# Kernel optimization log

Measured on AMD Instinct MI355X. Metric: run time of the kernel, lower is better.

The kernel has to match this reference:

```python
import jax, jax.numpy as jnp
import numpy as np

EMB = 1024
HEADS = 16
HEAD_DIM = EMB // HEADS


def setup_inputs() -> dict:
    key = jax.random.key(0)
    k1, k2, k3, k4 = jax.random.split(key, 4)
    x = jax.random.normal(k1, (4, 2048, EMB), dtype=jnp.float32)
    # torch Linear weight is [out, in]; store as [in, out] for x @ W
    W_qkv = jax.random.normal(k2, (EMB, 3 * EMB), dtype=jnp.float32) * (1.0 / np.sqrt(EMB))
    W_proj = jax.random.normal(k3, (EMB, EMB), dtype=jnp.float32) * (1.0 / np.sqrt(EMB))
    b_proj = jax.random.normal(k4, (EMB,), dtype=jnp.float32) * 0.01
    return {"x": x, "W_qkv": W_qkv, "W_proj": W_proj, "b_proj": b_proj}


def reference(x, W_qkv, W_proj, b_proj):
    B, S, D = x.shape
    H, hd = HEADS, HEAD_DIM
    qkv = x @ W_qkv                                  # [B,S,3D]
    q, k, v = jnp.split(qkv, 3, axis=-1)
    q = q.reshape(B, S, H, hd).transpose(0, 2, 1, 3)  # [B,H,S,hd]
    k = k.reshape(B, S, H, hd).transpose(0, 2, 1, 3)
    v = v.reshape(B, S, H, hd).transpose(0, 2, 1, 3)
    att = jnp.einsum('bhqd,bhkd->bhqk', q, k) * (1.0 / np.sqrt(hd))
    causal = jnp.tril(jnp.ones((S, S), dtype=bool))
    att = jnp.where(causal[None, None], att, jnp.float32(-jnp.inf))
    att = jax.nn.softmax(att, axis=-1)
    # dropout omitted (eval mode / deterministic baseline)
    out = jnp.einsum('bhqk,bhkd->bhqd', att, v)       # [B,H,S,hd]
    out = out.transpose(0, 2, 1, 3).reshape(B, S, D)
    return out @ W_proj + b_proj
```

## Files before the change

### kernel.cpp

```cpp
#include <hip/hip_runtime.h>
#include <math.h>

#define S_   2048
#define D_   1024
#define H_   16
#define HD_  64
#define BH_  64
#define TOK_ 8192

typedef __attribute__((ext_vector_type(8))) short  short8;
typedef __attribute__((ext_vector_type(4))) float  floatx4;

__device__ __forceinline__ short f2bf(float f) {
  union { float f; unsigned u; } c; c.f = f;
  unsigned u = c.u;
  u += 0x7fffu + ((u >> 16) & 1u);
  return (short)(u >> 16);
}

__device__ __forceinline__ void gload16(const void* g, void* l) {
  __builtin_amdgcn_global_load_lds((const __attribute__((address_space(1))) void*)g,
                                   (__attribute__((address_space(3))) void*)l, 16, 0, 0);
}

__global__ void cvt_x_kernel(const float* __restrict__ in, short* __restrict__ out, int n8) {
  int i = blockIdx.x * blockDim.x + threadIdx.x;
  if (i >= n8) return;
  const float4* p = (const float4*)in;
  float4 a = p[i * 2], b = p[i * 2 + 1];
  short8 o;
  o[0] = f2bf(a.x); o[1] = f2bf(a.y); o[2] = f2bf(a.z); o[3] = f2bf(a.w);
  o[4] = f2bf(b.x); o[5] = f2bf(b.y); o[6] = f2bf(b.z); o[7] = f2bf(b.w);
  ((short8*)out)[i] = o;
}

__global__ void tconv_kernel(const float* __restrict__ in, short* __restrict__ out, int R, int C) {
  __shared__ float t[32][33];
  int tx = threadIdx.x, ty = threadIdx.y;
  int c0 = blockIdx.x * 32, r0 = blockIdx.y * 32;
#pragma unroll
  for (int i = 0; i < 4; ++i)
    t[ty + i * 8][tx] = in[(r0 + ty + i * 8) * C + c0 + tx];
  __syncthreads();
#pragma unroll
  for (int i = 0; i < 4; ++i)
    out[(c0 + ty + i * 8) * R + r0 + tx] = f2bf(t[tx][ty + i * 8]);
}

__global__ void tv_kernel(const short* __restrict__ vb, short* __restrict__ vtb) {
  __shared__ short t[32][33];
  int tx = threadIdx.x, ty = threadIdx.y;
  int bh = blockIdx.z;
  int d0 = blockIdx.x * 32, s0 = blockIdx.y * 32;
  const short* src = vb + bh * S_ * HD_;
  short* dst = vtb + bh * HD_ * S_;
#pragma unroll
  for (int i = 0; i < 4; ++i)
    t[ty + i * 8][tx] = src[(s0 + ty + i * 8) * HD_ + d0 + tx];
  __syncthreads();
#pragma unroll
  for (int i = 0; i < 4; ++i)
    dst[(d0 + ty + i * 8) * S_ + s0 + tx] = t[tx][ty + i * 8];
}

__global__ __launch_bounds__(256) void gemm_qkv_kernel(
    const short* __restrict__ A, const short* __restrict__ Bt,
    short* __restrict__ qb, short* __restrict__ kb, short* __restrict__ vb) {
  __shared__ short sA[128 * 32];
  __shared__ short sB[128 * 32];
  const int tid = threadIdx.x;
  const int lane = tid & 63, wid = tid >> 6;
  const int wm = wid >> 1, wn = wid & 1;
  const int lr = lane & 15, lg = lane >> 4;
  const int m0 = blockIdx.x * 128, n0 = blockIdx.y * 128;
  floatx4 acc[4][4] = {};
  const int f1 = tid * 16;
  const int rS1 = f1 >> 6, cS1 = (f1 & 63) >> 1;
  const int f2 = f1 + 4096;
  const int rS2 = f2 >> 6, cS2 = (f2 & 63) >> 1;
  for (int kt = 0; kt < 32; ++kt) {
    const int k0 = kt * 32;
    __syncthreads();
    gload16(&A[(m0 + rS1) * 1024 + k0 + cS1], (char*)sA + f1);
    gload16(&A[(m0 + rS2) * 1024 + k0 + cS2], (char*)sA + f2);
    gload16(&Bt[(n0 + rS1) * 1024 + k0 + cS1], (char*)sB + f1);
    gload16(&Bt[(n0 + rS2) * 1024 + k0 + cS2], (char*)sB + f2);
    __syncthreads();
    short8 af[4], bfv[4];
#pragma unroll
    for (int mf = 0; mf < 4; ++mf)
      af[mf] = *(const short8*)&sA[(wm * 64 + mf * 16 + lr) * 32 + lg * 8];
#pragma unroll
    for (int nf = 0; nf < 4; ++nf)
      bfv[nf] = *(const short8*)&sB[(wn * 64 + nf * 16 + lr) * 32 + lg * 8];
#pragma unroll
    for (int mf = 0; mf < 4; ++mf)
#pragma unroll
      for (int nf = 0; nf < 4; ++nf)
        acc[mf][nf] = __builtin_amdgcn_mfma_f32_16x16x32_bf16(af[mf], bfv[nf], acc[mf][nf], 0, 0, 0);
  }
  const int sec = n0 >> 10;
  short* dst = sec == 0 ? qb : (sec == 1 ? kb : vb);
  const float scale = (sec == 0) ? 0.18033688011112042f : 1.0f;
#pragma unroll
  for (int mf = 0; mf < 4; ++mf) {
#pragma unroll
    for (int nf = 0; nf < 4; ++nf) {
      const int col = n0 + wn * 64 + nf * 16 + lr;
      const int w = col & 1023;
      const int h = w >> 6, d = w & 63;
#pragma unroll
      for (int r = 0; r < 4; ++r) {
        const int token = m0 + wm * 64 + mf * 16 + lg * 4 + r;
        const int b = token >> 11, s = token & 2047;
        dst[(((b << 4) | h) * 2048 + s) * 64 + d] = f2bf(acc[mf][nf][r] * scale);
      }
    }
  }
}

__global__ __launch_bounds__(256) void gemm_proj_kernel(
    const short* __restrict__ A, const short* __restrict__ Bt,
    const float* __restrict__ bias, float* __restrict__ out) {
  __shared__ short sA[128 * 32];
  __shared__ short sB[128 * 32];
  const int tid = threadIdx.x;
  const int lane = tid & 63, wid = tid >> 6;
  const int wm = wid >> 1, wn = wid & 1;
  const int lr = lane & 15, lg = lane >> 4;
  const int m0 = blockIdx.x * 128, n0 = blockIdx.y * 128;
  floatx4 acc[4][4] = {};
  const int f1 = tid * 16;
  const int rS1 = f1 >> 6, cS1 = (f1 & 63) >> 1;
  const int f2 = f1 + 4096;
  const int rS2 = f2 >> 6, cS2 = (f2 & 63) >> 1;
  for (int kt = 0; kt < 32; ++kt) {
    const int k0 = kt * 32;
    __syncthreads();
    gload16(&A[(m0 + rS1) * 1024 + k0 + cS1], (char*)sA + f1);
    gload16(&A[(m0 + rS2) * 1024 + k0 + cS2], (char*)sA + f2);
    gload16(&Bt[(n0 + rS1) * 1024 + k0 + cS1], (char*)sB + f1);
    gload16(&Bt[(n0 + rS2) * 1024 + k0 + cS2], (char*)sB + f2);
    __syncthreads();
    short8 af[4], bfv[4];
#pragma unroll
    for (int mf = 0; mf < 4; ++mf)
      af[mf] = *(const short8*)&sA[(wm * 64 + mf * 16 + lr) * 32 + lg * 8];
#pragma unroll
    for (int nf = 0; nf < 4; ++nf)
      bfv[nf] = *(const short8*)&sB[(wn * 64 + nf * 16 + lr) * 32 + lg * 8];
#pragma unroll
    for (int mf = 0; mf < 4; ++mf)
#pragma unroll
      for (int nf = 0; nf < 4; ++nf)
        acc[mf][nf] = __builtin_amdgcn_mfma_f32_16x16x32_bf16(af[mf], bfv[nf], acc[mf][nf], 0, 0, 0);
  }
#pragma unroll
  for (int mf = 0; mf < 4; ++mf) {
#pragma unroll
    for (int nf = 0; nf < 4; ++nf) {
      const int col = n0 + wn * 64 + nf * 16 + lr;
      const float bv = bias[col];
#pragma unroll
      for (int r = 0; r < 4; ++r) {
        const int row = m0 + wm * 64 + mf * 16 + lg * 4 + r;
        out[row * 1024 + col] = acc[mf][nf][r] + bv;
      }
    }
  }
}

__global__ __launch_bounds__(256) void attn_kernel(
    const short* __restrict__ qb, const short* __restrict__ kb,
    const short* __restrict__ vtb, short* __restrict__ attb) {
  __shared__ short sK[2][64 * 64];
  __shared__ short sVT[2][64 * 64];
  __shared__ short sP[4][32 * 64];
  const int tid = threadIdx.x;
  const int lane = tid & 63, wid = tid >> 6;
  const int lr = lane & 15, lg = lane >> 4;

  const int bid = blockIdx.x;
  const int wgid = (bid & 7) * 64 + (bid >> 3);
  const int bh = wgid >> 3;
  const int qx = wgid & 7;

  const char* kbase = (const char*)(kb + bh * S_ * HD_);
  const char* vtbase = (const char*)(vtb + bh * HD_ * S_);
  const short* qbase = qb + bh * S_ * HD_;
  char* pbase = (char*)&sP[wid][0];
  const int b = bh >> 4, h = bh & 15;

  const int f1 = tid * 16;
  const int ro1 = f1 >> 7, cb1 = f1 & 127;
  const int sc1 = cb1 ^ ((ro1 & 7) << 4);
  const int f2 = f1 + 4096;
  const int ro2 = f2 >> 7, cb2 = f2 & 127;
  const int sc2 = cb2 ^ ((ro2 & 7) << 4);

  const int swz = (lr & 7) << 4;

  short8 vones;
#pragma unroll
  for (int j = 0; j < 8; ++j) vones[j] = (short)0x3F80;

#pragma unroll 1
  for (int half = 0; half < 2; ++half) {
    const int qt = half ? (15 - qx) : qx;
    const int qw = qt * 128 + wid * 32;

    short8 qf[2][2];
#pragma unroll
    for (int qtile = 0; qtile < 2; ++qtile)
#pragma unroll
      for (int kf = 0; kf < 2; ++kf)
        qf[qtile][kf] = *(const short8*)&qbase[(qw + qtile * 16 + lr) * 64 + kf * 32 + lg * 8];

    floatx4 acc_o[2][4] = {};
    floatx4 acc_den[2] = {};
    float mrun[2] = {-1e30f, -1e30f};

    const int ntiles = 2 * qt + 2;

    {
      char* dK = (char*)sK[0];
      char* dV = (char*)sVT[0];
      gload16(kbase + ro1 * 128 + sc1, dK + f1);
      gload16(kbase + ro2 * 128 + sc2, dK + f2);
      gload16(vtbase + ro1 * 4096 + sc1, dV + f1);
      gload16(vtbase + ro2 * 4096 + sc2, dV + f2);
      asm volatile("s_waitcnt vmcnt(0)" ::: "memory");
      __builtin_amdgcn_s_barrier();
      __builtin_amdgcn_sched_barrier(0);
    }

    int cur = 0;
#pragma unroll 1
    for (int t = 0; t < ntiles; ++t) {
      if (t + 1 < ntiles) {
        const int key0n = (t + 1) * 64;
        char* dK = (char*)sK[cur ^ 1];
        char* dV = (char*)sVT[cur ^ 1];
        gload16(kbase + (key0n + ro1) * 128 + sc1, dK + f1);
        gload16(kbase + (key0n + ro2) * 128 + sc2, dK + f2);
        gload16(vtbase + ro1 * 4096 + key0n * 2 + sc1, dV + f1);
        gload16(vtbase + ro2 * 4096 + key0n * 2 + sc2, dV + f2);
      }
      const int key0 = t * 64;
      if (key0 <= qw + 31) {
        const char* cK = (const char*)sK[cur];
        const char* cV = (const char*)sVT[cur];

        floatx4 sT[4][2] = {};
        __builtin_amdgcn_s_setprio(1);
#pragma unroll
        for (int kt = 0; kt < 4; ++kt) {
#pragma unroll
          for (int kf = 0; kf < 2; ++kf) {
            short8 kfrag = *(const short8*)(cK + (kt * 16 + lr) * 128 + ((kf * 64 + lg * 16) ^ swz));
#pragma unroll
            for (int qtile = 0; qtile < 2; ++qtile)
              sT[kt][qtile] = __builtin_amdgcn_mfma_f32_16x16x32_bf16(kfrag, qf[qtile][kf], sT[kt][qtile], 0, 0, 0);
          }
        }
        __builtin_amdgcn_s_setprio(0);

        if (key0 + 63 > qw) {
#pragma unroll
          for (int kt = 0; kt < 4; ++kt)
#pragma unroll
            for (int qtile = 0; qtile < 2; ++qtile)
#pragma unroll
              for (int r = 0; r < 4; ++r)
                if (key0 + kt * 16 + lg * 4 + r > qw + qtile * 16 + lr) sT[kt][qtile][r] = -1e30f;
        }

        float mx[2], al[2];
        bool need = false;
#pragma unroll
        for (int qtile = 0; qtile < 2; ++qtile) {
          float m0v = fmaxf(fmaxf(sT[0][qtile][0], sT[0][qtile][1]), fmaxf(sT[0][qtile][2], sT[0][qtile][3]));
          float m1v = fmaxf(fmaxf(sT[1][qtile][0], sT[1][qtile][1]), fmaxf(sT[1][qtile][2], sT[1][qtile][3]));
          float m2v = fmaxf(fmaxf(sT[2][qtile][0], sT[2][qtile][1]), fmaxf(sT[2][qtile][2], sT[2][qtile][3]));
          float m3v = fmaxf(fmaxf(sT[3][qtile][0], sT[3][qtile][1]), fmaxf(sT[3][qtile][2], sT[3][qtile][3]));
          float m = fmaxf(fmaxf(m0v, m1v), fmaxf(m2v, m3v));
          m = fmaxf(m, __shfl_xor(m, 16));
          m = fmaxf(m, __shfl_xor(m, 32));
          mx[qtile] = m;
          need = need || (m > mrun[qtile] + 8.f);
        }
        if (__any(need)) {
#pragma unroll
          for (int qtile = 0; qtile < 2; ++qtile) {
            const float mnew = fmaxf(mrun[qtile], mx[qtile]);
            al[qtile] = __builtin_amdgcn_exp2f(mrun[qtile] - mnew);
            mrun[qtile] = mnew;
          }
#pragma unroll
          for (int mf = 0; mf < 2; ++mf) {
#pragma unroll
            for (int r = 0; r < 4; ++r) {
              const float alr = __shfl(al[mf], lg * 4 + r);
              acc_den[mf][r] *= alr;
#pragma unroll
              for (int nfd = 0; nfd < 4; ++nfd) acc_o[mf][nfd][r] *= alr;
            }
          }
        }

#pragma unroll
        for (int kt = 0; kt < 4; ++kt) {
#pragma unroll
          for (int qtile = 0; qtile < 2; ++qtile) {
            const float p0 = __builtin_amdgcn_exp2f(sT[kt][qtile][0] - mrun[qtile]);
            const float p1 = __builtin_amdgcn_exp2f(sT[kt][qtile][1] - mrun[qtile]);
            const float p2 = __builtin_amdgcn_exp2f(sT[kt][qtile][2] - mrun[qtile]);
            const float p3 = __builtin_amdgcn_exp2f(sT[kt][qtile][3] - mrun[qtile]);
            unsigned lo, hi;
            asm("v_cvt_pk_bf16_f32 %0, %1, %2" : "=v"(lo) : "v"(p0), "v"(p1));
            asm("v_cvt_pk_bf16_f32 %0, %1, %2" : "=v"(hi) : "v"(p2), "v"(p3));
            *(unsigned long long*)(pbase + (qtile * 16 + lr) * 128 + ((kt * 32 + lg * 8) ^ swz)) =
                ((unsigned long long)hi << 32) | lo;
          }
        }

        __builtin_amdgcn_s_setprio(1);
#pragma unroll
        for (int kf2 = 0; kf2 < 2; ++kf2) {
          short8 pf[2];
#pragma unroll
          for (int mf = 0; mf < 2; ++mf) {
            pf[mf] = *(const short8*)(pbase + (mf * 16 + lr) * 128 + ((kf2 * 64 + lg * 16) ^ swz));
            acc_den[mf] = __builtin_amdgcn_mfma_f32_16x16x32_bf16(pf[mf], vones, acc_den[mf], 0, 0, 0);
          }
#pragma unroll
          for (int nfd = 0; nfd < 4; ++nfd) {
            short8 vfrag = *(const short8*)(cV + (nfd * 16 + lr) * 128 + ((kf2 * 64 + lg * 16) ^ swz));
#pragma unroll
            for (int mf = 0; mf < 2; ++mf)
              acc_o[mf][nfd] = __builtin_amdgcn_mfma_f32_16x16x32_bf16(pf[mf], vfrag, acc_o[mf][nfd], 0, 0, 0);
          }
        }
        __builtin_amdgcn_s_setprio(0);
      }

      __builtin_amdgcn_sched_barrier(0);
      asm volatile("s_waitcnt vmcnt(0)" ::: "memory");
      __builtin_amdgcn_s_barrier();
      __builtin_amdgcn_sched_barrier(0);
      cur ^= 1;
    }

#pragma unroll
    for (int mf = 0; mf < 2; ++mf) {
#pragma unroll
      for (int nfd = 0; nfd < 4; ++nfd) {
#pragma unroll
        for (int r = 0; r < 4; ++r) {
          const float o = acc_o[mf][nfd][r] / acc_den[mf][r];
          const int qrow = qw + mf * 16 + lg * 4 + r;
          const int d = nfd * 16 + lr;
          attb[(b * 2048 + qrow) * 1024 + h * 64 + d] = f2bf(o);
        }
      }
    }
  }
}

extern "C" void kernel_launch(void* const* d_in, const int* in_sizes, int n_in,
                              void* d_out, int out_size, void* d_ws, size_t ws_size,
                              hipStream_t stream) {
  (void)in_sizes; (void)n_in; (void)out_size; (void)ws_size;
  const float* x = (const float*)d_in[0];
  const float* Wqkv = (const float*)d_in[1];
  const float* Wproj = (const float*)d_in[2];
  const float* bproj = (const float*)d_in[3];
  float* out = (float*)d_out;

  char* w = (char*)d_ws;
  short* xb     = (short*)(w + 0);
  short* wqkvT  = (short*)(w + 16777216);
  short* wprojT = (short*)(w + 23068672);
  short* qb     = (short*)(w + 25165824);
  short* kb     = (short*)(w + 41943040);
  short* vb     = (short*)(w + 58720256);
  short* vtb    = (short*)(w + 75497472);
  short* attb   = (short*)(w + 92274688);

  cvt_x_kernel<<<4096, 256, 0, stream>>>(x, xb, TOK_ * D_ / 8);
  tconv_kernel<<<dim3(96, 32), dim3(32, 8), 0, stream>>>(Wqkv, wqkvT, 1024, 3072);
  tconv_kernel<<<dim3(32, 32), dim3(32, 8), 0, stream>>>(Wproj, wprojT, 1024, 1024);
  gemm_qkv_kernel<<<dim3(64, 24), 256, 0, stream>>>(xb, wqkvT, qb, kb, vb);
  tv_kernel<<<dim3(2, 64, 64), dim3(32, 8), 0, stream>>>(vb, vtb);
  attn_kernel<<<512, 256, 0, stream>>>(qb, kb, vtb, attb);
  gemm_proj_kernel<<<dim3(64, 8), 256, 0, stream>>>(attb, wprojT, bproj, out);
}
```

Before: 262.2 us.

## Fuse V transpose into QKV GEMM epilogue and triple-buffer attention K/V loads

The QKV GEMM now writes V directly in transposed layout, using packed 8-byte stores of four consecutive tokens, which removes the separate tv_kernel launch and its round trip through memory. The attention kernel moves from double to triple buffering of K/V tiles in LDS, waiting with vmcnt(4) so that one tile load stays in flight while the current tile is computed, and it drops the trailing barrier. The row-max reduction uses v_max3_f32 to cut the instruction count. Costs are more LDS per block, which may lower occupancy, and a fragile hand-tuned wait count.

New measurement: 264.7 us. No clear change (+0.9%).

```diff
diff --git a/kernel.cpp b/kernel.cpp
--- a/kernel.cpp
+++ b/kernel.cpp
@@ -16,6 +16,10 @@
   unsigned u = c.u;
   u += 0x7fffu + ((u >> 16) & 1u);
   return (short)(u >> 16);
+}
+
+__device__ __forceinline__ float max3f(float a, float b, float c) {
+  float d; asm("v_max3_f32 %0, %1, %2, %3" : "=v"(d) : "v"(a), "v"(b), "v"(c)); return d;
 }
 
 __device__ __forceinline__ void gload16(const void* g, void* l) {
@@ -47,25 +51,9 @@
     out[(c0 + ty + i * 8) * R + r0 + tx] = f2bf(t[tx][ty + i * 8]);
 }
 
-__global__ void tv_kernel(const short* __restrict__ vb, short* __restrict__ vtb) {
-  __shared__ short t[32][33];
-  int tx = threadIdx.x, ty = threadIdx.y;
-  int bh = blockIdx.z;
-  int d0 = blockIdx.x * 32, s0 = blockIdx.y * 32;
-  const short* src = vb + bh * S_ * HD_;
-  short* dst = vtb + bh * HD_ * S_;
-#pragma unroll
-  for (int i = 0; i < 4; ++i)
-    t[ty + i * 8][tx] = src[(s0 + ty + i * 8) * HD_ + d0 + tx];
-  __syncthreads();
-#pragma unroll
-  for (int i = 0; i < 4; ++i)
-    dst[(d0 + ty + i * 8) * S_ + s0 + tx] = t[tx][ty + i * 8];
-}
-
 __global__ __launch_bounds__(256) void gemm_qkv_kernel(
     const short* __restrict__ A, const short* __restrict__ Bt,
-    short* __restrict__ qb, short* __restrict__ kb, short* __restrict__ vb) {
+    short* __restrict__ qb, short* __restrict__ kb, short* __restrict__ vtb) {
   __shared__ short sA[128 * 32];
   __shared__ short sB[128 * 32];
   const int tid = threadIdx.x;
@@ -100,20 +88,40 @@
         acc[mf][nf] = __builtin_amdgcn_mfma_f32_16x16x32_bf16(af[mf], bfv[nf], acc[mf][nf], 0, 0, 0);
   }
   const int sec = n0 >> 10;
-  short* dst = sec == 0 ? qb : (sec == 1 ? kb : vb);
-  const float scale = (sec == 0) ? 0.18033688011112042f : 1.0f;
-#pragma unroll
-  for (int mf = 0; mf < 4; ++mf) {
-#pragma unroll
-    for (int nf = 0; nf < 4; ++nf) {
-      const int col = n0 + wn * 64 + nf * 16 + lr;
-      const int w = col & 1023;
-      const int h = w >> 6, d = w & 63;
-#pragma unroll
-      for (int r = 0; r < 4; ++r) {
-        const int token = m0 + wm * 64 + mf * 16 + lg * 4 + r;
-        const int b = token >> 11, s = token & 2047;
-        dst[(((b << 4) | h) * 2048 + s) * 64 + d] = f2bf(acc[mf][nf][r] * scale);
+  if (sec < 2) {
+    short* dst = sec == 0 ? qb : kb;
+    const float scale = (sec == 0) ? 0.18033688011112042f : 1.0f;
+#pragma unroll
+    for (int mf = 0; mf < 4; ++mf) {
+#pragma unroll
+      for (int nf = 0; nf < 4; ++nf) {
+        const int col = n0 + wn * 64 + nf * 16 + lr;
+        const int w = col & 1023;
+        const int h = w >> 6, d = w & 63;
+#pragma unroll
+        for (int r = 0; r < 4; ++r) {
+          const int token = m0 + wm * 64 + mf * 16 + lg * 4 + r;
+          const int b = token >> 11, s = token & 2047;
+          dst[(((b << 4) | h) * 2048 + s) * 64 + d] = f2bf(acc[mf][nf][r] * scale);
+        }
+      }
+    }
+  } else {
+#pragma unroll
+    for (int mf = 0; mf < 4; ++mf) {
+      const int token0 = m0 + wm * 64 + mf * 16 + lg * 4;
+      const int bb = token0 >> 11, s0v = token0 & 2047;
+#pragma unroll
+      for (int nf = 0; nf < 4; ++nf) {
+        const int col = n0 + wn * 64 + nf * 16 + lr;
+        const int w = col & 1023;
+        const int h = w >> 6, d = w & 63;
+        union { unsigned long long u; short s[4]; } pk;
+        pk.s[0] = f2bf(acc[mf][nf][0]);
+        pk.s[1] = f2bf(acc[mf][nf][1]);
+        pk.s[2] = f2bf(acc[mf][nf][2]);
+        pk.s[3] = f2bf(acc[mf][nf][3]);
+        *(unsigned long long*)&vtb[((((bb << 4) | h) * 64 + d) << 11) + s0v] = pk.u;
       }
     }
   }
@@ -173,8 +181,8 @@
 __global__ __launch_bounds__(256) void attn_kernel(
     const short* __restrict__ qb, const short* __restrict__ kb,
     const short* __restrict__ vtb, short* __restrict__ attb) {
-  __shared__ short sK[2][64 * 64];
-  __shared__ short sVT[2][64 * 64];
+  __shared__ short sK[3][64 * 64];
+  __shared__ short sVT[3][64 * 64];
   __shared__ short sP[4][32 * 64];
   const int tid = threadIdx.x;
   const int lane = tid & 63, wid = tid >> 6;
@@ -222,30 +230,35 @@
 
     const int ntiles = 2 * qt + 2;
 
-    {
-      char* dK = (char*)sK[0];
-      char* dV = (char*)sVT[0];
-      gload16(kbase + ro1 * 128 + sc1, dK + f1);
-      gload16(kbase + ro2 * 128 + sc2, dK + f2);
-      gload16(vtbase + ro1 * 4096 + sc1, dV + f1);
-      gload16(vtbase + ro2 * 4096 + sc2, dV + f2);
-      asm volatile("s_waitcnt vmcnt(0)" ::: "memory");
+    __builtin_amdgcn_s_barrier();
+
+    const char* kp1 = kbase + ro1 * 128 + sc1;
+    const char* kp2 = kbase + ro2 * 128 + sc2;
+    const char* vp1 = vtbase + ro1 * 4096 + sc1;
+    const char* vp2 = vtbase + ro2 * 4096 + sc2;
+
+    gload16(kp1, (char*)sK[0] + f1);  gload16(kp2, (char*)sK[0] + f2);
+    gload16(vp1, (char*)sVT[0] + f1); gload16(vp2, (char*)sVT[0] + f2);
+    kp1 += 8192; kp2 += 8192; vp1 += 128; vp2 += 128;
+    gload16(kp1, (char*)sK[1] + f1);  gload16(kp2, (char*)sK[1] + f2);
+    gload16(vp1, (char*)sVT[1] + f1); gload16(vp2, (char*)sVT[1] + f2);
+    kp1 += 8192; kp2 += 8192; vp1 += 128; vp2 += 128;
+
+    int cur = 0, nxt2 = 2;
+#pragma unroll 1
+    for (int t = 0; t < ntiles; ++t) {
+      if (t < ntiles - 1) { asm volatile("s_waitcnt vmcnt(4)" ::: "memory"); }
+      else                { asm volatile("s_waitcnt vmcnt(0)" ::: "memory"); }
       __builtin_amdgcn_s_barrier();
       __builtin_amdgcn_sched_barrier(0);
-    }
-
-    int cur = 0;
-#pragma unroll 1
-    for (int t = 0; t < ntiles; ++t) {
-      if (t + 1 < ntiles) {
-        const int key0n = (t + 1) * 64;
-        char* dK = (char*)sK[cur ^ 1];
-        char* dV = (char*)sVT[cur ^ 1];
-        gload16(kbase + (key0n + ro1) * 128 + sc1, dK + f1);
-        gload16(kbase + (key0n + ro2) * 128 + sc2, dK + f2);
-        gload16(vtbase + ro1 * 4096 + key0n * 2 + sc1, dV + f1);
-        gload16(vtbase + ro2 * 4096 + key0n * 2 + sc2, dV + f2);
-      }
+      if (t + 2 < ntiles) {
+        char* dK = (char*)sK[nxt2];
+        char* dV = (char*)sVT[nxt2];
+        gload16(kp1, dK + f1);  gload16(kp2, dK + f2);
+        gload16(vp1, dV + f1);  gload16(vp2, dV + f2);
+      }
+      kp1 += 8192; kp2 += 8192; vp1 += 128; vp2 += 128;
+
       const int key0 = t * 64;
       if (key0 <= qw + 31) {
         const char* cK = (const char*)sK[cur];
@@ -279,11 +292,14 @@
         bool need = false;
 #pragma unroll
         for (int qtile = 0; qtile < 2; ++qtile) {
-          float m0v = fmaxf(fmaxf(sT[0][qtile][0], sT[0][qtile][1]), fmaxf(sT[0][qtile][2], sT[0][qtile][3]));
-          float m1v = fmaxf(fmaxf(sT[1][qtile][0], sT[1][qtile][1]), fmaxf(sT[1][qtile][2], sT[1][qtile][3]));
-          float m2v = fmaxf(fmaxf(sT[2][qtile][0], sT[2][qtile][1]), fmaxf(sT[2][qtile][2], sT[2][qtile][3]));
-          float m3v = fmaxf(fmaxf(sT[3][qtile][0], sT[3][qtile][1]), fmaxf(sT[3][qtile][2], sT[3][qtile][3]));
-          float m = fmaxf(fmaxf(m0v, m1v), fmaxf(m2v, m3v));
+          float m = max3f(sT[0][qtile][0], sT[0][qtile][1], sT[0][qtile][2]);
+          m = max3f(m, sT[0][qtile][3], sT[1][qtile][0]);
+          m = max3f(m, sT[1][qtile][1], sT[1][qtile][2]);
+          m = max3f(m, sT[1][qtile][3], sT[2][qtile][0]);
+          m = max3f(m, sT[2][qtile][1], sT[2][qtile][2]);
+          m = max3f(m, sT[2][qtile][3], sT[3][qtile][0]);
+          m = max3f(m, sT[3][qtile][1], sT[3][qtile][2]);
+          m = fmaxf(m, sT[3][qtile][3]);
           m = fmaxf(m, __shfl_xor(m, 16));
           m = fmaxf(m, __shfl_xor(m, 32));
           mx[qtile] = m;
@@ -344,11 +360,8 @@
         __builtin_amdgcn_s_setprio(0);
       }
 
-      __builtin_amdgcn_sched_barrier(0);
-      asm volatile("s_waitcnt vmcnt(0)" ::: "memory");
-      __builtin_amdgcn_s_barrier();
-      __builtin_amdgcn_sched_barrier(0);
-      cur ^= 1;
+      cur = (cur == 2) ? 0 : cur + 1;
+      nxt2 = (nxt2 == 2) ? 0 : nxt2 + 1;
     }
 
 #pragma unroll
@@ -383,15 +396,13 @@
   short* wprojT = (short*)(w + 23068672);
   short* qb     = (short*)(w + 25165824);
   short* kb     = (short*)(w + 41943040);
-  short* vb     = (short*)(w + 58720256);
   short* vtb    = (short*)(w + 75497472);
   short* attb   = (short*)(w + 92274688);
 
   cvt_x_kernel<<<4096, 256, 0, stream>>>(x, xb, TOK_ * D_ / 8);
   tconv_kernel<<<dim3(96, 32), dim3(32, 8), 0, stream>>>(Wqkv, wqkvT, 1024, 3072);
   tconv_kernel<<<dim3(32, 32), dim3(32, 8), 0, stream>>>(Wproj, wprojT, 1024, 1024);
-  gemm_qkv_kernel<<<dim3(64, 24), 256, 0, stream>>>(xb, wqkvT, qb, kb, vb);
-  tv_kernel<<<dim3(2, 64, 64), dim3(32, 8), 0, stream>>>(vb, vtb);
+  gemm_qkv_kernel<<<dim3(64, 24), 256, 0, stream>>>(xb, wqkvT, qb, kb, vtb);
   attn_kernel<<<512, 256, 0, stream>>>(qb, kb, vtb, attb);
   gemm_proj_kernel<<<dim3(64, 8), 256, 0, stream>>>(attb, wprojT, bproj, out);
 }
```
